# Kernel optimization log

Hardware: AMD Instinct MI355X
Metric: run time of the kernel (lower is better)

## Reference

```python
import jax, jax.numpy as jnp
import numpy as np

N = 50000   # nodes
E = 800000  # edges (avg degree 16)
H = 3       # attention heads
D_IN, D_HID, D_OUT = 256, 64, 10


def setup_inputs() -> dict:
    key = jax.random.key(0)
    ks = jax.random.split(key, 8)
    x = jax.random.normal(ks[0], (N, D_IN), dtype=jnp.float32)
    edge_index = jax.random.randint(ks[1], (2, E), 0, N, dtype=jnp.int64)
    W1 = jax.random.normal(ks[2], (H, D_IN, D_HID), dtype=jnp.float32) / np.sqrt(D_IN)
    a_src1 = jax.random.normal(ks[3], (H, D_HID), dtype=jnp.float32) / np.sqrt(D_HID)
    a_dst1 = jax.random.normal(ks[4], (H, D_HID), dtype=jnp.float32) / np.sqrt(D_HID)
    W2 = jax.random.normal(ks[5], (H, D_HID, D_OUT), dtype=jnp.float32) / np.sqrt(D_HID)
    a_src2 = jax.random.normal(ks[6], (H, D_OUT), dtype=jnp.float32) / np.sqrt(D_OUT)
    a_dst2 = jax.random.normal(ks[7], (H, D_OUT), dtype=jnp.float32) / np.sqrt(D_OUT)
    return {"x": x, "edge_index": edge_index, "W1": W1, "a_src1": a_src1,
            "a_dst1": a_dst1, "W2": W2, "a_src2": a_src2, "a_dst2": a_dst2}


def gat_layer(x, src, dst, W, a_s, a_d, n):
    # x: [N, Din]; W: [H, Din, Dout]; returns [N, Dout] (heads averaged)
    z = jnp.einsum('nd,hde->nhe', x, W)                     # [N, H, Dout]
    e_src = jnp.einsum('nhe,he->nh', z, a_s)[src]           # [E, H]
    e_dst = jnp.einsum('nhe,he->nh', z, a_d)[dst]           # [E, H]
    e = jax.nn.leaky_relu(e_src + e_dst, 0.2)               # [E, H]
    # numerically-stable softmax over incoming edges of each dst node
    m = jax.lax.stop_gradient(jax.ops.segment_max(e, dst, num_segments=n))
    ex = jnp.exp(e - m[dst])                                # [E, H]
    denom = jax.ops.segment_sum(ex, dst, num_segments=n)    # [N, H]
    alpha = ex / (denom[dst] + 1e-16)                       # [E, H]
    out = jax.ops.segment_sum(z[src] * alpha[:, :, None], dst, num_segments=n)
    return out.mean(axis=1)                                 # [N, Dout]


def reference(x, edge_index, W1, a_src1, a_dst1, W2, a_src2, a_dst2):
    n = x.shape[0]
    src, dst = edge_index[0], edge_index[1]
    # dropout layers are identity in eval/deterministic mode
    h = gat_layer(x, src, dst, W1, a_src1, a_dst1, n)
    h = jax.nn.elu(h)
    h = gat_layer(h, src, dst, W2, a_src2, a_dst2, n)
    return h, jax.nn.log_softmax(h, axis=1)
```

## Files before the change

kernel.cpp:

```cpp
#include <hip/hip_runtime.h>
#include <math.h>

#define DIN  256
#define DHID 64
#define NH   3
#define DOUT 10
#define CAP  64

typedef __attribute__((ext_vector_type(8))) short bf16x8;
typedef __attribute__((ext_vector_type(4))) float f32x4;

__device__ inline unsigned short f2bf(float f) {
    unsigned u = __builtin_bit_cast(unsigned, f);
    unsigned r = (u + 0x7FFFu + ((u >> 16) & 1u)) >> 16;
    return (unsigned short)r;
}
__device__ inline float bf2f(unsigned short s) {
    unsigned u = ((unsigned)s) << 16;
    return __builtin_bit_cast(float, u);
}
__device__ inline f32x4 cvt4(ushort4 z) {
    f32x4 r;
    r[0] = bf2f(z.x); r[1] = bf2f(z.y); r[2] = bf2f(z.z); r[3] = bf2f(z.w);
    return r;
}


__global__ __launch_bounds__(256) void repack_zero_kernel(const float* __restrict__ W1,
                                                          const float* __restrict__ W2,
                                                          unsigned short* __restrict__ W1p,
                                                          float* __restrict__ W2catT,
                                                          int* __restrict__ cursor, int N) {
    int bid = blockIdx.x;
    int tid = threadIdx.x;
    int nzb = (N + 255) >> 8;
    if (bid < 192) {
        int idx = bid * 256 + tid;
        int j = idx & 7, l = (idx >> 3) & 63, q = (idx >> 9) & 7, t = idx >> 12;
        int c = t * 16 + (l & 15);
        int k = q * 32 + (l >> 4) * 8 + j;
        int h = c >> 6, jj = c & 63;
        W1p[idx] = f2bf(W1[h * 16384 + k * 64 + jj]);
    } else if (bid < 192 + nzb) {
        int i = (bid - 192) * 256 + tid;
        if (i < N) cursor[i] = 0;
    } else {
        int idx = (bid - 192 - nzb) * 256 + tid;
        if (idx < 2048) {
            int cc = idx >> 6, kk = idx & 63;
            float wv = 0.f;
            if (cc < 30) {
                int h = cc / 10, j = cc % 10;
                wv = W2[(h * 64 + kk) * 10 + j];
            }
            W2catT[idx] = wv;
        }
    }
}


#define SCHUNK 2048

__global__ __launch_bounds__(256) void scatter_kernel(const int* __restrict__ src,
                                                      const int* __restrict__ dst,
                                                      int* __restrict__ cursor,
                                                      unsigned short* __restrict__ esrcp,
                                                      int E, int pbase) {
    int part = blockIdx.x & 7;
    int base = (blockIdx.x >> 3) * SCHUNK;
    int tid = threadIdx.x;
    int lo = part * pbase, hi = lo + pbase;
    #pragma unroll
    for (int k = 0; k < SCHUNK / 256; ++k) {
        int i = base + k * 256 + tid;
        if (i < E) {
            int d = dst[i];
            int s = src[i];
            if (d >= lo && d < hi) {
                int pos = atomicAdd(cursor + d, 1);
                if (pos < CAP) esrcp[d * CAP + pos] = (unsigned short)s;
            }
        }
    }
}


__global__ __launch_bounds__(128) void gemm1_mfma_kernel(const float* __restrict__ x,
                                                         const bf16x8* __restrict__ W1p,
                                                         const float* __restrict__ a_s,
                                                         const float* __restrict__ a_d,
                                                         unsigned short* __restrict__ z1bf,
                                                         float* __restrict__ s1,
                                                         float* __restrict__ d1, int n) {
    __shared__ unsigned short Xs[32][272];
    int tid = threadIdx.x;
    int w = tid >> 6, lane = tid & 63;
    int m = lane & 15, quad = lane >> 4;
    int n0 = blockIdx.x * 32;

    for (int i = tid; i < 2048; i += 128) {
        int r = i >> 6, c4 = i & 63;
        int nn = n0 + r;
        float4 a = (nn < n) ? *(const float4*)(x + (size_t)nn * 256 + c4 * 4)
                            : (float4){0.f, 0.f, 0.f, 0.f};
        ushort4 b;
        b.x = f2bf(a.x); b.y = f2bf(a.y); b.z = f2bf(a.z); b.w = f2bf(a.w);
        *(ushort4*)(&Xs[r][c4 * 4]) = b;
    }
    __syncthreads();

    int rloc = w * 16 + m;
    f32x4 acc[12];
    #pragma unroll
    for (int t = 0; t < 12; ++t) acc[t] = (f32x4){0.f, 0.f, 0.f, 0.f};
    #pragma unroll
    for (int q = 0; q < 8; ++q) {
        bf16x8 af = *(const bf16x8*)(&Xs[rloc][q * 32 + quad * 8]);
        #pragma unroll
        for (int t = 0; t < 12; ++t) {
            bf16x8 bfr = W1p[(t * 8 + q) * 64 + lane];
            acc[t] = __builtin_amdgcn_mfma_f32_16x16x32_bf16(af, bfr, acc[t], 0, 0, 0);
        }
    }
    __syncthreads();

    float as_r[12], ad_r[12];
    #pragma unroll
    for (int t = 0; t < 12; ++t) { as_r[t] = a_s[t * 16 + m]; ad_r[t] = a_d[t * 16 + m]; }

    #pragma unroll
    for (int reg = 0; reg < 4; ++reg) {
        int row_loc = w * 16 + quad * 4 + reg;
        int row_out = n0 + row_loc;
        bool ok = row_out < n;
        float ps[3] = {0.f, 0.f, 0.f}, pd[3] = {0.f, 0.f, 0.f};
        #pragma unroll
        for (int t = 0; t < 12; ++t) {
            float v = acc[t][reg];
            Xs[row_loc][t * 16 + m] = f2bf(v);
            ps[t >> 2] += v * as_r[t];
            pd[t >> 2] += v * ad_r[t];
        }
        #pragma unroll
        for (int h = 0; h < 3; ++h) {
            float s = ps[h], d = pd[h];
            #pragma unroll
            for (int msk = 1; msk < 16; msk <<= 1) {
                s += __shfl_xor(s, msk, 16);
                d += __shfl_xor(d, msk, 16);
            }
            if (ok && m == 0) { s1[row_out * 4 + h] = s; d1[row_out * 4 + h] = d; }
        }
    }
    __syncthreads();

    for (int i = tid; i < 1536; i += 128) {
        int r = i / 48, c4 = i % 48;
        int nn = n0 + r;
        if (nn < n)
            *(ushort4*)(z1bf + (size_t)nn * 192 + c4 * 4) = *(const ushort4*)(&Xs[r][c4 * 4]);
    }
}


#define CONSUME8(Z, OFF)                                              \
    {                                                                 \
        f32x4 wa4 = *(const f32x4*)(&wl[wb + (OFF)]);                 \
        f32x4 wb4 = *(const f32x4*)(&wl[wb + (OFF) + 4]);             \
        acc += cvt4(Z[0]) * wa4[0]; acc += cvt4(Z[1]) * wa4[1];       \
        acc += cvt4(Z[2]) * wa4[2]; acc += cvt4(Z[3]) * wa4[3];       \
        acc += cvt4(Z[4]) * wb4[0]; acc += cvt4(Z[5]) * wb4[1];       \
        acc += cvt4(Z[6]) * wb4[2]; acc += cvt4(Z[7]) * wb4[3];       \
    }

__global__ __launch_bounds__(256) void agg1_gemm2_kernel(
        const int* __restrict__ cnts, const unsigned short* __restrict__ esrcp,
        const float* __restrict__ s1, const float* __restrict__ d1,
        const unsigned short* __restrict__ z1bf,
        const float* __restrict__ W2catT, const float* __restrict__ as2,
        const float* __restrict__ ad2,
        unsigned short* __restrict__ z2bf,
        float* __restrict__ s2, float* __restrict__ d2, int n) {
    __shared__ float wlds[4][204];
    __shared__ float hb[4][64];
    __shared__ float tb[4][64];
    int tid = threadIdx.x;
    int lane = tid & 63, wave = tid >> 6;
    int v = blockIdx.x * 4 + wave;
    if (v >= n) return;
    int cnt = cnts[v]; if (cnt > CAP) cnt = CAP;
    int m16 = lane & 15;
    int grp = lane >> 4;
    int head = grp > 2 ? 2 : grp;
    int c = lane & 31, half = lane >> 5;
    bool rowact = lane < 48;
    const int wb = head * 68;
    float* wl = wlds[wave];

    int u_l = 0;
    if (lane < cnt) u_l = (int)esrcp[v * CAP + lane];

    ushort4 zA[8], zB[8];
    if (rowact) {
        #pragma unroll
        for (int i = 0; i < 8; ++i) {
            int u = __builtin_amdgcn_readlane(u_l, i);
            zA[i] = *(const ushort4*)(z1bf + (size_t)u * 192 + lane * 4);
        }
        #pragma unroll
        for (int i = 0; i < 8; ++i) {
            int u = __builtin_amdgcn_readlane(u_l, 8 + i);
            zB[i] = *(const ushort4*)(z1bf + (size_t)u * 192 + lane * 4);
        }
    }

    f32x4 wsr[8];
    #pragma unroll
    for (int j2 = 0; j2 < 8; ++j2)
        wsr[j2] = *(const f32x4*)(W2catT + (c << 6) + (half << 5) + (j2 << 2));

    float dv0 = d1[v * 4], dv1 = d1[v * 4 + 1], dv2 = d1[v * 4 + 2];
    float w0 = 0.f, w1 = 0.f, w2 = 0.f;
    if (lane < cnt) {
        float4 sv = *(const float4*)(s1 + (size_t)u_l * 4);
        float e0 = sv.x + dv0; e0 = e0 > 0.f ? e0 : 0.2f * e0;
        float e1 = sv.y + dv1; e1 = e1 > 0.f ? e1 : 0.2f * e1;
        float e2 = sv.z + dv2; e2 = e2 > 0.f ? e2 : 0.2f * e2;
        w0 = __expf(e0); w1 = __expf(e1); w2 = __expf(e2);
    }
    wl[lane] = w0; wl[68 + lane] = w1; wl[136 + lane] = w2;

    int rnd = (cnt + 7) & ~7; if (rnd < 16) rnd = 16;
    f32x4 acc = (f32x4){0.f, 0.f, 0.f, 0.f};
    if (rowact) {
        int jc = 0;
        for (int js = 16; js < rnd; js += 8) {
            ushort4 zN[8];
            #pragma unroll
            for (int i = 0; i < 8; ++i) {
                int u = __builtin_amdgcn_readlane(u_l, js + i);
                zN[i] = *(const ushort4*)(z1bf + (size_t)u * 192 + lane * 4);
            }
            CONSUME8(zA, jc); jc += 8;
            #pragma unroll
            for (int i = 0; i < 8; ++i) { zA[i] = zB[i]; zB[i] = zN[i]; }
        }
        CONSUME8(zA, jc);
        CONSUME8(zB, jc + 8);
    }

    f32x4 wv4 = *(const f32x4*)(&wl[head * 68 + m16 * 4]);
    float denp = wv4[0] + wv4[1] + wv4[2] + wv4[3];
    #pragma unroll
    for (int msk = 1; msk < 16; msk <<= 1) denp += __shfl_xor(denp, msk, 16);

    float invd = (1.f / 3.f) / (denp + 1e-16f);
    float acc0 = rowact ? acc[0] * invd : 0.f;
    float acc1 = rowact ? acc[1] * invd : 0.f;
    float acc2 = rowact ? acc[2] * invd : 0.f;
    float acc3 = rowact ? acc[3] * invd : 0.f;
    acc0 += __shfl_down(acc0, 32, 64); acc0 += __shfl_down(acc0, 16, 64);
    acc1 += __shfl_down(acc1, 32, 64); acc1 += __shfl_down(acc1, 16, 64);
    acc2 += __shfl_down(acc2, 32, 64); acc2 += __shfl_down(acc2, 16, 64);
    acc3 += __shfl_down(acc3, 32, 64); acc3 += __shfl_down(acc3, 16, 64);
    if (lane < 16) {
        float4 o;
        o.x = acc0 > 0.f ? acc0 : __expf(acc0) - 1.f;
        o.y = acc1 > 0.f ? acc1 : __expf(acc1) - 1.f;
        o.z = acc2 > 0.f ? acc2 : __expf(acc2) - 1.f;
        o.w = acc3 > 0.f ? acc3 : __expf(acc3) - 1.f;
        *(float4*)(&hb[wave][lane * 4]) = o;
    }

    f32x4 accW = (f32x4){0.f, 0.f, 0.f, 0.f};
    #pragma unroll
    for (int j2 = 0; j2 < 8; ++j2) {
        f32x4 h4 = *(const f32x4*)(&hb[wave][(half << 5) + (j2 << 2)]);
        accW += h4 * wsr[j2];
    }
    float zc = accW[0] + accW[1] + accW[2] + accW[3];
    zc += __shfl_down(zc, 32, 64);
    if (lane < 32) {
        z2bf[(size_t)v * 32 + c] = f2bf(zc);
        if (c < 30) {
            tb[wave][c]      = zc * as2[c];
            tb[wave][32 + c] = zc * ad2[c];
        }
    }
    if (lane < 6) {
        int h = lane >> 1;
        int base = (lane & 1) * 32 + h * 10;
        float sum = 0.f;
        #pragma unroll
        for (int j = 0; j < 10; ++j) sum += tb[wave][base + j];
        if ((lane & 1) == 0) s2[v * 4 + h] = sum;
        else                 d2[v * 4 + h] = sum;
    }
}


__global__ __launch_bounds__(256) void agg2_kernel(const int* __restrict__ cnts,
                                                   const unsigned short* __restrict__ esrcp,
                                                   const float* __restrict__ s2,
                                                   const float* __restrict__ d2,
                                                   const unsigned short* __restrict__ z2bf,
                                                   float* __restrict__ out, int n) {
    __shared__ float wlds[4][196];
    __shared__ float dlds[4][4];
    int tid = threadIdx.x;
    int lane = tid & 63, wave = tid >> 6;
    int v = blockIdx.x * 4 + wave;
    if (v >= n) return;
    int cnt = cnts[v]; if (cnt > CAP) cnt = CAP;
    int c2 = lane & 15;
    int quad = lane >> 4;
    int headc = c2 < 5 ? 0 : (c2 < 10 ? 1 : 2);
    int headg = quad > 2 ? 2 : quad;
    float dv0 = d2[v * 4], dv1 = d2[v * 4 + 1], dv2 = d2[v * 4 + 2];
    float* wl = wlds[wave];

    int u_l = 0; float w0 = 0.f, w1 = 0.f, w2 = 0.f;
    if (lane < cnt) {
        u_l = (int)esrcp[v * CAP + lane];
        float4 sv = *(const float4*)(s2 + (size_t)u_l * 4);
        float e0 = sv.x + dv0; e0 = e0 > 0.f ? e0 : 0.2f * e0;
        float e1 = sv.y + dv1; e1 = e1 > 0.f ? e1 : 0.2f * e1;
        float e2 = sv.z + dv2; e2 = e2 > 0.f ? e2 : 0.2f * e2;
        w0 = __expf(e0); w1 = __expf(e1); w2 = __expf(e2);
    }
    wl[lane] = w0; wl[65 + lane] = w1; wl[130 + lane] = w2;

    float ax = 0.f, ay = 0.f;
    {
        int rnd = (cnt + 7) & ~7;
        const int wb = headc * 65;
        int ua = __shfl(u_l, quad, 64);
        int ub = __shfl(u_l, 4 + quad, 64);
        float wa = wl[wb + quad], wbb = wl[wb + 4 + quad];
        ushort2 za = *(const ushort2*)(z2bf + (size_t)ua * 32 + c2 * 2);
        ushort2 zb = *(const ushort2*)(z2bf + (size_t)ub * 32 + c2 * 2);
        for (int j = 8; j < rnd; j += 8) {
            int un1 = __shfl(u_l, j + quad, 64);
            int un2 = __shfl(u_l, j + 4 + quad, 64);
            float wn1 = wl[wb + j + quad], wn2 = wl[wb + j + 4 + quad];
            ushort2 zn1 = *(const ushort2*)(z2bf + (size_t)un1 * 32 + c2 * 2);
            ushort2 zn2 = *(const ushort2*)(z2bf + (size_t)un2 * 32 + c2 * 2);
            ax += wa * bf2f(za.x) + wbb * bf2f(zb.x);
            ay += wa * bf2f(za.y) + wbb * bf2f(zb.y);
            wa = wn1; wbb = wn2; za = zn1; zb = zn2;
        }
        ax += wa * bf2f(za.x) + wbb * bf2f(zb.x);
        ay += wa * bf2f(za.y) + wbb * bf2f(zb.y);
    }

    float4 wv = *(const float4*)(&wl[headg * 65 + c2 * 4]);
    float denp = wv.x + wv.y + wv.z + wv.w;
    #pragma unroll
    for (int msk = 1; msk < 16; msk <<= 1) denp += __shfl_xor(denp, msk, 16);
    if (c2 == 0 && quad < 3) dlds[wave][quad] = denp;
    float den = dlds[wave][headc];

    ax += __shfl_down(ax, 32, 64); ax += __shfl_down(ax, 16, 64);
    ay += __shfl_down(ay, 32, 64); ay += __shfl_down(ay, 16, 64);
    float inv = 1.f / (den + 1e-16f);
    float rx = ax * inv, ry = ay * inv;
    float rx5  = __shfl(rx, lane + 5, 64);
    float rx10 = __shfl(rx, lane + 10, 64);
    float ry5  = __shfl(ry, lane + 5, 64);
    float ry10 = __shfl(ry, lane + 10, 64);
    float rrx = (rx + rx5 + rx10) * (1.f / 3.f);
    float rry = (ry + ry5 + ry10) * (1.f / 3.f);
    bool act = lane < 5;
    float mx = act ? fmaxf(rrx, rry) : -1e30f;
    #pragma unroll
    for (int msk = 1; msk < 8; msk <<= 1) mx = fmaxf(mx, __shfl_xor(mx, msk, 8));
    float e = act ? (__expf(rrx - mx) + __expf(rry - mx)) : 0.f;
    #pragma unroll
    for (int msk = 1; msk < 8; msk <<= 1) e += __shfl_xor(e, msk, 8);
    float lg = __logf(e);
    if (act) {
        float2 o1; o1.x = rrx; o1.y = rry;
        float2 o2; o2.x = rrx - mx - lg; o2.y = rry - mx - lg;
        *(float2*)(out + (size_t)v * DOUT + c2 * 2) = o1;
        *(float2*)(out + (size_t)n * DOUT + (size_t)v * DOUT + c2 * 2) = o2;
    }
}


extern "C" void kernel_launch(void* const* d_in, const int* in_sizes, int n_in,
                              void* d_out, int out_size, void* d_ws, size_t ws_size,
                              hipStream_t stream) {
    const float* x   = (const float*)d_in[0];
    const int*   ei  = (const int*)d_in[1];
    const float* W1  = (const float*)d_in[2];
    const float* as1 = (const float*)d_in[3];
    const float* ad1 = (const float*)d_in[4];
    const float* W2  = (const float*)d_in[5];
    const float* as2 = (const float*)d_in[6];
    const float* ad2 = (const float*)d_in[7];
    float* out = (float*)d_out;

    const int N = in_sizes[0] / DIN;
    const int E = in_sizes[1] / 2;
    const int* src = ei;
    const int* dst = ei + E;

    char* p = (char*)d_ws;
    auto alloc = [&](size_t bytes) -> void* {
        void* r = (void*)p;
        p += (bytes + 255) & ~(size_t)255;
        return r;
    };
    int* cursor  = (int*)alloc((size_t)N * 4);
    unsigned short* esrcp = (unsigned short*)alloc((size_t)N * CAP * 2);
    unsigned short* W1p  = (unsigned short*)alloc((size_t)49152 * 2);
    float* W2catT = (float*)alloc((size_t)2048 * 4);
    unsigned short* z1bf = (unsigned short*)alloc((size_t)N * 192 * 2);
    float* s1    = (float*)alloc((size_t)N * 4 * 4);
    float* d1    = (float*)alloc((size_t)N * 4 * 4);
    unsigned short* z2bf = (unsigned short*)alloc((size_t)N * 32 * 2);
    float* s2    = (float*)alloc((size_t)N * 4 * 4);
    float* d2    = (float*)alloc((size_t)N * 4 * 4);
    (void)alloc(512);

    int nzb = (N + 255) / 256;
    repack_zero_kernel<<<192 + nzb + 8, 256, 0, stream>>>(W1, W2, W1p, W2catT, cursor, N);

    int pbase = (N + 7) / 8;
    int nchunks = (E + SCHUNK - 1) / SCHUNK;
    scatter_kernel<<<nchunks * 8, 256, 0, stream>>>(src, dst, cursor, esrcp, E, pbase);

    gemm1_mfma_kernel<<<(N + 31) / 32, 128, 0, stream>>>(x, (const bf16x8*)W1p, as1, ad1,
                                                         z1bf, s1, d1, N);
    agg1_gemm2_kernel<<<(N + 3) / 4, 256, 0, stream>>>(cursor, esrcp, s1, d1, z1bf,
                                                       W2catT, as2, ad2, z2bf, s2, d2, N);
    agg2_kernel<<<(N + 3) / 4, 256, 0, stream>>>(cursor, esrcp, s2, d2, z2bf, out, N);
}
```

Baseline: 275.6 us.

## Merge edge scatter into GEMM1 launch and shrink agg1 prefetch pipeline

The edge bucketing scatter and the first-layer GEMM are independent, so both now run in one launch. The first S blocks do the scatter and the rest do the GEMM, which removes a kernel boundary and lets the two workloads overlap. The agg1 kernel's neighbour-feature pipeline drops from a two-deep prefetch to a single-deep one, and the W2 weight registers are no longer preloaded but read at use time. These changes cut register pressure so more waves can be resident, at the cost of less load latency hiding per wave. The scatter also loads src only for edges in the block's partition.

```diff
diff --git a/kernel.cpp b/kernel.cpp
--- a/kernel.cpp
+++ b/kernel.cpp
@@ -58,45 +58,45 @@
     }
 }
 
-
 #define SCHUNK 2048
 
-__global__ __launch_bounds__(256) void scatter_kernel(const int* __restrict__ src,
-                                                      const int* __restrict__ dst,
-                                                      int* __restrict__ cursor,
-                                                      unsigned short* __restrict__ esrcp,
-                                                      int E, int pbase) {
-    int part = blockIdx.x & 7;
-    int base = (blockIdx.x >> 3) * SCHUNK;
-    int tid = threadIdx.x;
-    int lo = part * pbase, hi = lo + pbase;
-    #pragma unroll
-    for (int k = 0; k < SCHUNK / 256; ++k) {
-        int i = base + k * 256 + tid;
-        if (i < E) {
-            int d = dst[i];
-            int s = src[i];
-            if (d >= lo && d < hi) {
-                int pos = atomicAdd(cursor + d, 1);
-                if (pos < CAP) esrcp[d * CAP + pos] = (unsigned short)s;
+
+__global__ __launch_bounds__(128) void gemm1_scatter_kernel(const float* __restrict__ x,
+                                                            const bf16x8* __restrict__ W1p,
+                                                            const float* __restrict__ a_s,
+                                                            const float* __restrict__ a_d,
+                                                            unsigned short* __restrict__ z1bf,
+                                                            float* __restrict__ s1,
+                                                            float* __restrict__ d1, int n,
+                                                            const int* __restrict__ src,
+                                                            const int* __restrict__ dst,
+                                                            int* __restrict__ cursor,
+                                                            unsigned short* __restrict__ esrcp,
+                                                            int E, int S, int pbase) {
+    __shared__ unsigned short Xs[32][272];
+    if ((int)blockIdx.x < S) {
+        int part = blockIdx.x & 7;
+        int base = ((int)blockIdx.x >> 3) * SCHUNK;
+        int lo = part * pbase, hi = lo + pbase;
+        #pragma unroll
+        for (int k = 0; k < SCHUNK / 128; ++k) {
+            int i = base + k * 128 + (int)threadIdx.x;
+            if (i < E) {
+                int d = dst[i];
+                if (d >= lo && d < hi) {
+                    int s = src[i];
+                    int pos = atomicAdd(cursor + d, 1);
+                    if (pos < CAP) esrcp[d * CAP + pos] = (unsigned short)s;
+                }
             }
         }
-    }
-}
-
-
-__global__ __launch_bounds__(128) void gemm1_mfma_kernel(const float* __restrict__ x,
-                                                         const bf16x8* __restrict__ W1p,
-                                                         const float* __restrict__ a_s,
-                                                         const float* __restrict__ a_d,
-                                                         unsigned short* __restrict__ z1bf,
-                                                         float* __restrict__ s1,
-                                                         float* __restrict__ d1, int n) {
-    __shared__ unsigned short Xs[32][272];
+        return;
+    }
+
     int tid = threadIdx.x;
     int w = tid >> 6, lane = tid & 63;
     int m = lane & 15, quad = lane >> 4;
-    int n0 = blockIdx.x * 32;
+    int n0 = (blockIdx.x - S) * 32;
 
     for (int i = tid; i < 2048; i += 128) {
         int r = i >> 6, c4 = i & 63;
@@ -162,16 +162,6 @@
     }
 }
 
-
-#define CONSUME8(Z, OFF)                                              \
-    {                                                                 \
-        f32x4 wa4 = *(const f32x4*)(&wl[wb + (OFF)]);                 \
-        f32x4 wb4 = *(const f32x4*)(&wl[wb + (OFF) + 4]);             \
-        acc += cvt4(Z[0]) * wa4[0]; acc += cvt4(Z[1]) * wa4[1];       \
-        acc += cvt4(Z[2]) * wa4[2]; acc += cvt4(Z[3]) * wa4[3];       \
-        acc += cvt4(Z[4]) * wb4[0]; acc += cvt4(Z[5]) * wb4[1];       \
-        acc += cvt4(Z[6]) * wb4[2]; acc += cvt4(Z[7]) * wb4[3];       \
-    }
 
 __global__ __launch_bounds__(256) void agg1_gemm2_kernel(
         const int* __restrict__ cnts, const unsigned short* __restrict__ esrcp,
@@ -192,36 +182,14 @@
     int m16 = lane & 15;
     int grp = lane >> 4;
     int head = grp > 2 ? 2 : grp;
-    int c = lane & 31, half = lane >> 5;
     bool rowact = lane < 48;
     const int wb = head * 68;
     float* wl = wlds[wave];
 
-    int u_l = 0;
-    if (lane < cnt) u_l = (int)esrcp[v * CAP + lane];
-
-    ushort4 zA[8], zB[8];
-    if (rowact) {
-        #pragma unroll
-        for (int i = 0; i < 8; ++i) {
-            int u = __builtin_amdgcn_readlane(u_l, i);
-            zA[i] = *(const ushort4*)(z1bf + (size_t)u * 192 + lane * 4);
-        }
-        #pragma unroll
-        for (int i = 0; i < 8; ++i) {
-            int u = __builtin_amdgcn_readlane(u_l, 8 + i);
-            zB[i] = *(const ushort4*)(z1bf + (size_t)u * 192 + lane * 4);
-        }
-    }
-
-    f32x4 wsr[8];
-    #pragma unroll
-    for (int j2 = 0; j2 < 8; ++j2)
-        wsr[j2] = *(const f32x4*)(W2catT + (c << 6) + (half << 5) + (j2 << 2));
-
     float dv0 = d1[v * 4], dv1 = d1[v * 4 + 1], dv2 = d1[v * 4 + 2];
-    float w0 = 0.f, w1 = 0.f, w2 = 0.f;
+    int u_l = 0; float w0 = 0.f, w1 = 0.f, w2 = 0.f;
     if (lane < cnt) {
+        u_l = (int)esrcp[v * CAP + lane];
         float4 sv = *(const float4*)(s1 + (size_t)u_l * 4);
         float e0 = sv.x + dv0; e0 = e0 > 0.f ? e0 : 0.2f * e0;
         float e1 = sv.y + dv1; e1 = e1 > 0.f ? e1 : 0.2f * e1;
@@ -230,23 +198,38 @@
     }
     wl[lane] = w0; wl[68 + lane] = w1; wl[136 + lane] = w2;
 
-    int rnd = (cnt + 7) & ~7; if (rnd < 16) rnd = 16;
     f32x4 acc = (f32x4){0.f, 0.f, 0.f, 0.f};
     if (rowact) {
-        int jc = 0;
-        for (int js = 16; js < rnd; js += 8) {
-            ushort4 zN[8];
+        int rnd = (cnt + 7) & ~7;
+        ushort4 zr[8];
+        #pragma unroll
+        for (int i = 0; i < 8; ++i) {
+            int u = __builtin_amdgcn_readlane(u_l, i);
+            zr[i] = *(const ushort4*)(z1bf + (size_t)u * 192 + lane * 4);
+        }
+        f32x4 wra = *(const f32x4*)(&wl[wb]);
+        f32x4 wrb = *(const f32x4*)(&wl[wb + 4]);
+        for (int j = 8; j < rnd; j += 8) {
+            ushort4 zn[8];
             #pragma unroll
             for (int i = 0; i < 8; ++i) {
-                int u = __builtin_amdgcn_readlane(u_l, js + i);
-                zN[i] = *(const ushort4*)(z1bf + (size_t)u * 192 + lane * 4);
+                int u = __builtin_amdgcn_readlane(u_l, j + i);
+                zn[i] = *(const ushort4*)(z1bf + (size_t)u * 192 + lane * 4);
             }
-            CONSUME8(zA, jc); jc += 8;
+            f32x4 wna = *(const f32x4*)(&wl[wb + j]);
+            f32x4 wnb = *(const f32x4*)(&wl[wb + j + 4]);
+            acc += cvt4(zr[0]) * wra[0]; acc += cvt4(zr[1]) * wra[1];
+            acc += cvt4(zr[2]) * wra[2]; acc += cvt4(zr[3]) * wra[3];
+            acc += cvt4(zr[4]) * wrb[0]; acc += cvt4(zr[5]) * wrb[1];
+            acc += cvt4(zr[6]) * wrb[2]; acc += cvt4(zr[7]) * wrb[3];
             #pragma unroll
-            for (int i = 0; i < 8; ++i) { zA[i] = zB[i]; zB[i] = zN[i]; }
-        }
-        CONSUME8(zA, jc);
-        CONSUME8(zB, jc + 8);
+            for (int i = 0; i < 8; ++i) zr[i] = zn[i];
+            wra = wna; wrb = wnb;
+        }
+        acc += cvt4(zr[0]) * wra[0]; acc += cvt4(zr[1]) * wra[1];
+        acc += cvt4(zr[2]) * wra[2]; acc += cvt4(zr[3]) * wra[3];
+        acc += cvt4(zr[4]) * wrb[0]; acc += cvt4(zr[5]) * wrb[1];
+        acc += cvt4(zr[6]) * wrb[2]; acc += cvt4(zr[7]) * wrb[3];
     }
 
     f32x4 wv4 = *(const f32x4*)(&wl[head * 68 + m16 * 4]);
@@ -272,11 +255,13 @@
         *(float4*)(&hb[wave][lane * 4]) = o;
     }
 
+    int c = lane & 31, half = lane >> 5;
+    const f32x4* wp = (const f32x4*)(W2catT + (c << 6) + (half << 5));
     f32x4 accW = (f32x4){0.f, 0.f, 0.f, 0.f};
     #pragma unroll
     for (int j2 = 0; j2 < 8; ++j2) {
         f32x4 h4 = *(const f32x4*)(&hb[wave][(half << 5) + (j2 << 2)]);
-        accW += h4 * wsr[j2];
+        accW += h4 * wp[j2];
     }
     float zc = accW[0] + accW[1] + accW[2] + accW[3];
     zc += __shfl_down(zc, 32, 64);
@@ -427,11 +412,12 @@
     repack_zero_kernel<<<192 + nzb + 8, 256, 0, stream>>>(W1, W2, W1p, W2catT, cursor, N);
 
     int pbase = (N + 7) / 8;
-    int nchunks = (E + SCHUNK - 1) / SCHUNK;
-    scatter_kernel<<<nchunks * 8, 256, 0, stream>>>(src, dst, cursor, esrcp, E, pbase);
-
-    gemm1_mfma_kernel<<<(N + 31) / 32, 128, 0, stream>>>(x, (const bf16x8*)W1p, as1, ad1,
-                                                         z1bf, s1, d1, N);
+    int S = ((E + SCHUNK - 1) / SCHUNK) * 8;
+    int G = (N + 31) / 32;
+    gemm1_scatter_kernel<<<S + G, 128, 0, stream>>>(x, (const bf16x8*)W1p, as1, ad1,
+                                                    z1bf, s1, d1, N,
+                                                    src, dst, cursor, esrcp, E, S, pbase);
+
     agg1_gemm2_kernel<<<(N + 3) / 4, 256, 0, stream>>>(cursor, esrcp, s1, d1, z1bf,
                                                        W2catT, as2, ad2, z2bf, s2, d2, N);
     agg2_kernel<<<(N + 3) / 4, 256, 0, stream>>>(cursor, esrcp, s2, d2, z2bf, out, N);
```

Result: slower. 289.5 us (+5.0%).
